# Kernel optimization log

Hardware: AMD Instinct MI355X
Metric: run time of the kernel (lower is better)

The kernel has to match this reference:

```python
import jax, jax.numpy as jnp
import numpy as np

HIDDEN = 64
NUM_LAYERS = 6
BN_EPS = 1e-5


def setup_inputs() -> dict:
    key = jax.random.key(0)
    N, M = 1024, 1024
    num_nodes = N + M
    ks = jax.random.split(key, 12)
    x = jax.random.normal(ks[0], (num_nodes, 2), dtype=jnp.float32)
    # complete bipartite edges: (a, N+b) for all a in [0,N), b in [0,M), row-major so view(N,M) is meaningful
    row = jnp.repeat(jnp.arange(N, dtype=jnp.int64), M)
    col = N + jnp.tile(jnp.arange(M, dtype=jnp.int64), N)
    edge_index = jnp.stack([row, col], axis=0)
    s = 1.0 / np.sqrt(HIDDEN)
    return {
        "x": x,
        "edge_index": edge_index,
        "in_w": jax.random.normal(ks[1], (2, HIDDEN), jnp.float32) * 0.5,
        "in_b": jnp.zeros((HIDDEN,), jnp.float32),
        "conv_w": jax.random.normal(ks[2], (NUM_LAYERS, HIDDEN, HIDDEN), jnp.float32) * s,
        "conv_b": jnp.zeros((NUM_LAYERS, HIDDEN), jnp.float32),
        "bn_gamma": jnp.ones((NUM_LAYERS, HIDDEN), jnp.float32),
        "bn_beta": jnp.zeros((NUM_LAYERS, HIDDEN), jnp.float32),
        "out_w": jax.random.normal(ks[3], (2 * HIDDEN, 1), jnp.float32) * s,
        "out_b": jnp.zeros((1,), jnp.float32),
        "N": N,
        "M": M,
    }


def reference(x, edge_index, in_w, in_b, conv_w, conv_b, bn_gamma, bn_beta, out_w, out_b, N, M):
    num_nodes = x.shape[0]
    # GCN normalization with added self-loops (PyG GCNConv defaults)
    loops = jnp.arange(num_nodes, dtype=edge_index.dtype)
    row = jnp.concatenate([edge_index[0], loops])
    col = jnp.concatenate([edge_index[1], loops])
    deg = jax.ops.segment_sum(jnp.ones_like(col, dtype=x.dtype), col, num_segments=num_nodes)
    dinv = jnp.where(deg > 0, jax.lax.rsqrt(deg), 0.0)
    norm = dinv[row] * dinv[col]  # [E+num_nodes]

    h = jax.nn.relu(x @ in_w + in_b)
    for i in range(NUM_LAYERS):
        h_res = h
        hw = h @ conv_w[i]
        agg = jax.ops.segment_sum(hw[row] * norm[:, None], col, num_segments=num_nodes)
        h = agg + conv_b[i]
        # BatchNorm1d in training mode: batch stats, biased variance
        mu = h.mean(axis=0)
        var = ((h - mu) ** 2).mean(axis=0)
        h = (h - mu) * jax.lax.rsqrt(var + BN_EPS) * bn_gamma[i] + bn_beta[i]
        h = jax.nn.relu(h)
        if i > 0 and i % 2 == 1:
            h = h + h_res

    ef = jnp.concatenate([h[edge_index[0]], h[edge_index[1]]], axis=1)  # [E, 2H]
    scores = (ef @ out_w + out_b)[:, 0]
    return scores.reshape(N, M)
```

## Files before the change

kernel.cpp:

```cpp
#include <hip/hip_runtime.h>


#define NBLK 64
#define MAGIC 0x13572468u

__device__ __forceinline__ float relu_(float x) { return x > 0.f ? x : 0.f; }

#define AT_LOAD(p)    __hip_atomic_load((p), __ATOMIC_RELAXED, __HIP_MEMORY_SCOPE_AGENT)
#define AT_STORE(p,v) __hip_atomic_store((p), (v), __ATOMIC_RELAXED, __HIP_MEMORY_SCOPE_AGENT)
#define AT_ADD(p,v)   __hip_atomic_fetch_add((p), (v), __ATOMIC_RELAXED, __HIP_MEMORY_SCOPE_AGENT)

#define PART_OFF  256
#define UV_OFF    12544
#define FLAG_OFF  14592

__global__ __launch_bounds__(256, 1) void k_fused(
    const float* __restrict__ x,
    const float* __restrict__ in_w, const float* __restrict__ in_b,
    const float* __restrict__ conv_w,
    const float* __restrict__ bn_g, const float* __restrict__ bn_b,
    const float* __restrict__ out_w, const float* __restrict__ out_b,
    float* __restrict__ out,
    unsigned int* __restrict__ ws)
{
    __shared__ float Wl[2][4096];
    __shared__ float hl[32 * 68];
    __shared__ float sredS[4 * 64], sredQ[4 * 64];
    __shared__ float pcoef[64], scoef[64];
    __shared__ float g_lds[384], b_lds[384];
    __shared__ float ow_lds[128];
    __shared__ float u_l[16];

    const int t = threadIdx.x, b = blockIdx.x;
    const int nl = t >> 3;
    const int fi = t & 7;
    const int f0 = fi * 8;
    const int node = b * 32 + nl;
    const bool isA = b < 32;
    float* part = (float*)(ws + PART_OFF);
    float* uv   = (float*)(ws + UV_OFF);

    {
        const float4* src = (const float4*)conv_w;
        float4* dst = (float4*)Wl[0];
        dst[t]       = src[t];
        dst[t + 256] = src[t + 256];
        dst[t + 512] = src[t + 512];
        dst[t + 768] = src[t + 768];
        for (int i = t; i < 384; i += 256) { g_lds[i] = bn_g[i]; b_lds[i] = bn_b[i]; }
        if (t < 128) ow_lds[t] = out_w[t];
    }

    if (b == 0) {
        for (int i = t; i < 224; i += 256) AT_STORE(ws + i, 0u);
        for (int i = t; i < 12288; i += 256) AT_STORE((unsigned*)part + i, 0u);
        asm volatile("s_waitcnt vmcnt(0)" ::: "memory");
        __syncthreads();
        if (t == 0) AT_STORE(ws + FLAG_OFF, MAGIC);
    }

    {
        float x0 = x[node * 2], x1 = x[node * 2 + 1];
#pragma unroll
        for (int j = 0; j < 8; j++) {
            int f = f0 + j;
            hl[nl * 68 + f] = relu_(fmaf(x0, in_w[f], fmaf(x1, in_w[64 + f], in_b[f])));
        }
    }
    __syncthreads();

    for (int layer = 0; layer < 6; layer++) {
        const float* Wb = Wl[layer & 1];
        float acc[8];
#pragma unroll
        for (int j = 0; j < 8; j++) acc[j] = 0.f;

#pragma unroll 4
        for (int k = 0; k < 64; k += 4) {
            float4 hh = *(const float4*)&hl[nl * 68 + k];
            float hv[4] = {hh.x, hh.y, hh.z, hh.w};
#pragma unroll
            for (int j = 0; j < 4; j++) {
                const float* wr = Wb + (k + j) * 64 + f0;
                float4 w0 = *(const float4*)wr;
                float4 w1 = *(const float4*)(wr + 4);
                float wv[8] = {w0.x, w0.y, w0.z, w0.w, w1.x, w1.y, w1.z, w1.w};
#pragma unroll
                for (int q = 0; q < 8; q++) acc[q] = fmaf(hv[j], wv[q], acc[q]);
            }
        }

        {
            float sv[8], qv[8];
#pragma unroll
            for (int j = 0; j < 8; j++) { sv[j] = acc[j]; qv[j] = acc[j] * acc[j]; }
#pragma unroll
            for (int m = 8; m < 64; m <<= 1) {
#pragma unroll
                for (int j = 0; j < 8; j++) {
                    sv[j] += __shfl_xor(sv[j], m);
                    qv[j] += __shfl_xor(qv[j], m);
                }
            }
            int w = t >> 6, lane = t & 63;
            if (lane < 8) {
#pragma unroll
                for (int j = 0; j < 8; j++) {
                    sredS[w * 64 + lane * 8 + j] = sv[j];
                    sredQ[w * 64 + lane * 8 + j] = qv[j];
                }
            }
        }
        if (layer == 0) {
            __syncthreads();
            if (t == 0) while (AT_LOAD(ws + FLAG_OFF) != MAGIC) {}
        }
        __syncthreads();

        if (t < 64) {
            float S = sredS[t] + sredS[64 + t] + sredS[128 + t] + sredS[192 + t];
            float Q = sredQ[t] + sredQ[64 + t] + sredQ[128 + t] + sredQ[192 + t];
            float* base = part + layer * 2048 + (b & 7) * 256 + (isA ? 0 : 128);
            AT_ADD(base + t, S);
            AT_ADD(base + 64 + t, Q);
        }

        asm volatile("s_waitcnt vmcnt(0)" ::: "memory");
        __syncthreads();
        if (t == 0) AT_ADD(ws + layer * 32, 1u);

        float4 pf0, pf1, pf2, pf3;
        if (layer < 5) {
            const float4* src = (const float4*)(conv_w + (layer + 1) * 4096);
            pf0 = src[t];
            pf1 = src[t + 256];
            pf2 = src[t + 512];
            pf3 = src[t + 768];
        }

        if (t == 0) {
            const unsigned int* c = ws + layer * 32;
            for (;;) {
                unsigned a0 = AT_LOAD(c);
                unsigned a1 = AT_LOAD(c);
                unsigned a2 = AT_LOAD(c);
                unsigned a3 = AT_LOAD(c);
                if (a0 >= NBLK) break;
                if (a1 >= NBLK) break;
                if (a2 >= NBLK) break;
                if (a3 >= NBLK) break;
            }
        }
        __syncthreads();

        if (layer < 5) {
            float4* dst = (float4*)Wl[(layer + 1) & 1];
            dst[t]       = pf0;
            dst[t + 256] = pf1;
            dst[t + 512] = pf2;
            dst[t + 768] = pf3;
        }

        if (t < 64) {
            const float* base = part + layer * 2048;
            float SA = 0.f, QA = 0.f, SB = 0.f, QB = 0.f;
#pragma unroll
            for (int r = 0; r < 8; r++) {
                const float* rb = base + r * 256;
                SA += AT_LOAD(rb + t);
                QA += AT_LOAD(rb + 64 + t);
                SB += AT_LOAD(rb + 128 + t);
                QB += AT_LOAD(rb + 192 + t);
            }
            const float c1 = 9.75609756097561e-4f;
            const float c2 = 3.1234752377721214e-2f;
            float sumAgg = SA + c1 * SB + 1024.f * c2 * SA;
            float sumSq  = QA + c1 * c1 * QB + 2.f * c1 * c2 * SA * SB
                         + 1024.f * c2 * c2 * SA * SA;
            float meanAgg = sumAgg * (1.f / 2048.f);
            float var = sumSq * (1.f / 2048.f) - meanAgg * meanAgg;
            float rstd = rsqrtf(var + 1e-5f);
            float scale = rstd * g_lds[layer * 64 + t];
            float bt = b_lds[layer * 64 + t];
            if (isA) { pcoef[t] = scale;      scoef[t] = bt - meanAgg * scale; }
            else     { pcoef[t] = c1 * scale; scoef[t] = bt + (c2 * SA - meanAgg) * scale; }
        }
        __syncthreads();

        float vals[8];
#pragma unroll
        for (int j = 0; j < 8; j++)
            vals[j] = relu_(fmaf(acc[j], pcoef[f0 + j], scoef[f0 + j]));
        if (layer == 1 || layer == 3 || layer == 5) {
#pragma unroll
            for (int j = 0; j < 8; j++) vals[j] += hl[nl * 68 + f0 + j];
        }

        if (layer < 5) {
#pragma unroll
            for (int j = 0; j < 8; j++) hl[nl * 68 + f0 + j] = vals[j];
            __syncthreads();
        } else {
            const float* w = ow_lds + (isA ? 0 : 64) + f0;
            float d = 0.f;
#pragma unroll
            for (int j = 0; j < 8; j++) d = fmaf(vals[j], w[j], d);
            d += __shfl_xor(d, 1);
            d += __shfl_xor(d, 2);
            d += __shfl_xor(d, 4);
            if (fi == 0) AT_STORE(uv + node, d);
        }
    }

    asm volatile("s_waitcnt vmcnt(0)" ::: "memory");
    __syncthreads();
    if (t == 0) {
        unsigned int* c = ws + 6 * 32;
        AT_ADD(c, 1u);
        for (;;) {
            unsigned a0 = AT_LOAD(c);
            unsigned a1 = AT_LOAD(c);
            unsigned a2 = AT_LOAD(c);
            unsigned a3 = AT_LOAD(c);
            if (a0 >= NBLK) break;
            if (a1 >= NBLK) break;
            if (a2 >= NBLK) break;
            if (a3 >= NBLK) break;
        }
    }
    __syncthreads();

    {
        if (t < 16) u_l[t] = AT_LOAD(uv + b * 16 + t);
        float ob = out_b[0];
        float4 vv;
        vv.x = AT_LOAD(uv + 1024 + 4 * t)     + ob;
        vv.y = AT_LOAD(uv + 1024 + 4 * t + 1) + ob;
        vv.z = AT_LOAD(uv + 1024 + 4 * t + 2) + ob;
        vv.w = AT_LOAD(uv + 1024 + 4 * t + 3) + ob;
        __syncthreads();
#pragma unroll
        for (int r = 0; r < 16; r++) {
            int a = b * 16 + r;
            float ua = u_l[r];
            ((float4*)(out + a * 1024))[t] =
                make_float4(ua + vv.x, ua + vv.y, ua + vv.z, ua + vv.w);
        }
    }
}

extern "C" void kernel_launch(void* const* d_in, const int* in_sizes, int n_in,
                              void* d_out, int out_size, void* d_ws, size_t ws_size,
                              hipStream_t stream) {
    const float* x      = (const float*)d_in[0];
    const float* in_w   = (const float*)d_in[2];
    const float* in_b   = (const float*)d_in[3];
    const float* conv_w = (const float*)d_in[4];
    const float* bn_g   = (const float*)d_in[6];
    const float* bn_b   = (const float*)d_in[7];
    const float* out_w  = (const float*)d_in[8];
    const float* out_b  = (const float*)d_in[9];
    float* out = (float*)d_out;

    k_fused<<<NBLK, 256, 0, stream>>>(x, in_w, in_b, conv_w, bn_g, bn_b,
                                      out_w, out_b, out, (unsigned int*)d_ws);
}
```

Baseline: 115.7 us.

## Split output broadcast into separate wide kernel and parallelize BN stat reduction

The final grid-wide barrier and the 4 MB outer-sum output write move out of the 64-block persistent kernel into a second kernel launched with 1024 blocks. The intent is to spread the output store over all CUs instead of only 64. The per-layer BatchNorm partial-sum reduction is also spread across all 256 threads into shared memory, rather than done by 64 threads each loading four values. This costs an extra kernel launch and one more __syncthreads per layer.

```diff
diff --git a/kernel.cpp b/kernel.cpp
--- a/kernel.cpp
+++ b/kernel.cpp
@@ -19,17 +19,16 @@
     const float* __restrict__ in_w, const float* __restrict__ in_b,
     const float* __restrict__ conv_w,
     const float* __restrict__ bn_g, const float* __restrict__ bn_b,
-    const float* __restrict__ out_w, const float* __restrict__ out_b,
-    float* __restrict__ out,
+    const float* __restrict__ out_w,
     unsigned int* __restrict__ ws)
 {
     __shared__ float Wl[2][4096];
     __shared__ float hl[32 * 68];
     __shared__ float sredS[4 * 64], sredQ[4 * 64];
+    __shared__ float stat[256];
     __shared__ float pcoef[64], scoef[64];
     __shared__ float g_lds[384], b_lds[384];
     __shared__ float ow_lds[128];
-    __shared__ float u_l[16];
 
     const int t = threadIdx.x, b = blockIdx.x;
     const int nl = t >> 3;
@@ -52,7 +51,7 @@
     }
 
     if (b == 0) {
-        for (int i = t; i < 224; i += 256) AT_STORE(ws + i, 0u);
+        for (int i = t; i < 192; i += 256) AT_STORE(ws + i, 0u);
         for (int i = t; i < 12288; i += 256) AT_STORE((unsigned*)part + i, 0u);
         asm volatile("s_waitcnt vmcnt(0)" ::: "memory");
         __syncthreads();
@@ -153,6 +152,15 @@
         }
         __syncthreads();
 
+        {
+            int item = t;
+            const float* p = part + layer * 2048 + item;
+            float s = 0.f;
+#pragma unroll
+            for (int r = 0; r < 8; r++) s += AT_LOAD(p + r * 256);
+            stat[item] = s;
+        }
+
         if (layer < 5) {
             float4* dst = (float4*)Wl[(layer + 1) & 1];
             dst[t]       = pf0;
@@ -160,18 +168,10 @@
             dst[t + 512] = pf2;
             dst[t + 768] = pf3;
         }
+        __syncthreads();
 
         if (t < 64) {
-            const float* base = part + layer * 2048;
-            float SA = 0.f, QA = 0.f, SB = 0.f, QB = 0.f;
-#pragma unroll
-            for (int r = 0; r < 8; r++) {
-                const float* rb = base + r * 256;
-                SA += AT_LOAD(rb + t);
-                QA += AT_LOAD(rb + 64 + t);
-                SB += AT_LOAD(rb + 128 + t);
-                QB += AT_LOAD(rb + 192 + t);
-            }
+            float SA = stat[t], QA = stat[64 + t], SB = stat[128 + t], QB = stat[192 + t];
             const float c1 = 9.75609756097561e-4f;
             const float c2 = 3.1234752377721214e-2f;
             float sumAgg = SA + c1 * SB + 1024.f * c2 * SA;
@@ -211,42 +211,17 @@
             if (fi == 0) AT_STORE(uv + node, d);
         }
     }
-
-    asm volatile("s_waitcnt vmcnt(0)" ::: "memory");
-    __syncthreads();
-    if (t == 0) {
-        unsigned int* c = ws + 6 * 32;
-        AT_ADD(c, 1u);
-        for (;;) {
-            unsigned a0 = AT_LOAD(c);
-            unsigned a1 = AT_LOAD(c);
-            unsigned a2 = AT_LOAD(c);
-            unsigned a3 = AT_LOAD(c);
-            if (a0 >= NBLK) break;
-            if (a1 >= NBLK) break;
-            if (a2 >= NBLK) break;
-            if (a3 >= NBLK) break;
-        }
-    }
-    __syncthreads();
-
-    {
-        if (t < 16) u_l[t] = AT_LOAD(uv + b * 16 + t);
-        float ob = out_b[0];
-        float4 vv;
-        vv.x = AT_LOAD(uv + 1024 + 4 * t)     + ob;
-        vv.y = AT_LOAD(uv + 1024 + 4 * t + 1) + ob;
-        vv.z = AT_LOAD(uv + 1024 + 4 * t + 2) + ob;
-        vv.w = AT_LOAD(uv + 1024 + 4 * t + 3) + ob;
-        __syncthreads();
-#pragma unroll
-        for (int r = 0; r < 16; r++) {
-            int a = b * 16 + r;
-            float ua = u_l[r];
-            ((float4*)(out + a * 1024))[t] =
-                make_float4(ua + vv.x, ua + vv.y, ua + vv.z, ua + vv.w);
-        }
-    }
+}
+
+__global__ __launch_bounds__(256) void k_out(const float* __restrict__ uv,
+                                             const float* __restrict__ out_b,
+                                             float* __restrict__ out) {
+    const int a = blockIdx.x;
+    const int t = threadIdx.x;
+    float ua = uv[a] + out_b[0];
+    float4 vv = ((const float4*)(uv + 1024))[t];
+    ((float4*)(out + a * 1024))[t] =
+        make_float4(ua + vv.x, ua + vv.y, ua + vv.z, ua + vv.w);
 }
 
 extern "C" void kernel_launch(void* const* d_in, const int* in_sizes, int n_in,
@@ -262,6 +237,10 @@
     const float* out_b  = (const float*)d_in[9];
     float* out = (float*)d_out;
 
+    unsigned int* ws = (unsigned int*)d_ws;
+    const float* uv = (const float*)(ws + UV_OFF);
+
     k_fused<<<NBLK, 256, 0, stream>>>(x, in_w, in_b, conv_w, bn_g, bn_b,
-                                      out_w, out_b, out, (unsigned int*)d_ws);
+                                      out_w, ws);
+    k_out<<<1024, 256, 0, stream>>>(uv, out_b, out);
 }
```

Result: no change. 113.8 us (-1.6%).
